# Optimization experiments

Hardware: AMD Instinct MI355X
Metric: run time of the kernel (lower is better)

The kernel has to match this reference:

```python
import jax, jax.numpy as jnp
import numpy as np

# Architecture constants (from module defaults)
D, H, DH, P, G, DEPTH, M, NCLS = 192, 3, 64, 16, 14, 12, 128, 1000  # M = feature_map_dim // 2
EXITS = (4, 8, 12)
TEMP = 1.0 / np.sqrt(DH)  # Favor softmax_temp = 1/sqrt(d_head)
EPS_ATTN = 1e-6           # fast_transformers LinearAttention eps
LN_EPS = 1e-5


def ln(x, g, b):
    mu = x.mean(-1, keepdims=True)
    var = ((x - mu) ** 2).mean(-1, keepdims=True)
    return (x - mu) * jax.lax.rsqrt(var + LN_EPS) * g + b


def favor(x, omega):
    # FAVOR+ positive random features for the softmax kernel.
    # x: [B,L,H,DH], omega: [DH,M] -> phi: [B,L,H,2M]
    xs = x * np.float32(np.sqrt(TEMP))
    off = 0.5 * (xs * xs).sum(-1, keepdims=True)
    u = jnp.einsum('blhd,dm->blhm', xs, omega)
    phi = jnp.concatenate([jnp.exp(u - off), jnp.exp(-u - off)], axis=-1)
    return phi * np.float32(1.0 / np.sqrt(2 * M))


def forward(x, patch_w, patch_b, pe_ln_g, pe_ln_b, cls_token, pos_embed,
            Wq, bq, Wk, bk, Wv, bv, Wo, bo,
            ln1_g, ln1_b, ln2_g, ln2_b, lnb_g, lnb_b,
            W1, b1, W2, b2, omega, head_w, head_b):
    B = x.shape[0]
    # Patch embedding: Conv2d(k=16, s=16) == blocked einsum
    xp = x.reshape(B, 3, G, P, G, P)
    tok = jnp.einsum('bchpwq,dcpq->bhwd', xp, patch_w).reshape(B, G * G, D) + patch_b
    tok = ln(tok, pe_ln_g, pe_ln_b)  # PatchEmbed.norm (norm_layer=LayerNorm)
    tok = jnp.concatenate([jnp.broadcast_to(cls_token, (B, 1, D)), tok], axis=1) + pos_embed
    xc = tok  # [B, 197, D]
    outs = []
    for i in range(DEPTH):
        # --- linear (FAVOR) attention ---
        q = (xc @ Wq[i].T + bq[i]).reshape(B, -1, H, DH)
        k = (xc @ Wk[i].T + bk[i]).reshape(B, -1, H, DH)
        v = (xc @ Wv[i].T + bv[i]).reshape(B, -1, H, DH)
        Qp = favor(q, omega[i])
        Kp = favor(k, omega[i])
        KV = jnp.einsum('bshm,bshd->bhmd', Kp, v)
        Z = 1.0 / (jnp.einsum('blhm,bhm->blh', Qp, Kp.sum(axis=1)) + EPS_ATTN)
        attn = jnp.einsum('blhm,bhmd,blh->blhd', Qp, KV, Z).reshape(B, -1, D)
        # fast_transformers TransformerEncoderLayer (post-norm style)
        xc = xc + attn @ Wo[i].T + bo[i]
        y = xc = ln(xc, ln1_g[i], ln1_b[i])
        y = jax.nn.relu(y @ W1[i].T + b1[i]) @ W2[i].T + b2[i]
        xc = ln(xc + y, ln2_g[i], ln2_b[i])
        # per-block TransformerEncoder final norm (builder final_normalization)
        xc = ln(xc, lnb_g[i], lnb_b[i])
        if (i + 1) in EXITS:
            j = EXITS.index(i + 1)
            z = xc.mean(axis=1)  # AdaptiveAvgPool1d(1) over sequence
            outs.append(z @ head_w[j].T + head_b[j])
    return tuple(outs)


def setup_inputs() -> dict:
    key = jax.random.key(0)
    ks = iter(jax.random.split(key, 32))
    n = lambda shape, s=0.02: jax.random.normal(next(ks), shape, jnp.float32) * s
    return dict(
        x=jax.random.normal(next(ks), (64, 3, 224, 224), jnp.float32),
        patch_w=n((D, 3, P, P)), patch_b=jnp.zeros((D,), jnp.float32),
        pe_ln_g=jnp.ones((D,), jnp.float32), pe_ln_b=jnp.zeros((D,), jnp.float32),
        cls_token=n((1, 1, D)), pos_embed=n((1, G * G + 1, D)),
        Wq=n((DEPTH, D, D)), bq=jnp.zeros((DEPTH, D), jnp.float32),
        Wk=n((DEPTH, D, D)), bk=jnp.zeros((DEPTH, D), jnp.float32),
        Wv=n((DEPTH, D, D)), bv=jnp.zeros((DEPTH, D), jnp.float32),
        Wo=n((DEPTH, D, D)), bo=jnp.zeros((DEPTH, D), jnp.float32),
        ln1_g=jnp.ones((DEPTH, D), jnp.float32), ln1_b=jnp.zeros((DEPTH, D), jnp.float32),
        ln2_g=jnp.ones((DEPTH, D), jnp.float32), ln2_b=jnp.zeros((DEPTH, D), jnp.float32),
        lnb_g=jnp.ones((DEPTH, D), jnp.float32), lnb_b=jnp.zeros((DEPTH, D), jnp.float32),
        W1=n((DEPTH, 4 * D, D)), b1=jnp.zeros((DEPTH, 4 * D), jnp.float32),
        W2=n((DEPTH, D, 4 * D)), b2=jnp.zeros((DEPTH, D), jnp.float32),
        omega=jax.random.normal(next(ks), (DEPTH, DH, M), jnp.float32),
        head_w=n((len(EXITS), NCLS, D)), head_b=jnp.zeros((len(EXITS), NCLS), jnp.float32),
    )


def reference(x, patch_w, patch_b, pe_ln_g, pe_ln_b, cls_token, pos_embed,
              Wq, bq, Wk, bk, Wv, bv, Wo, bo,
              ln1_g, ln1_b, ln2_g, ln2_b, lnb_g, lnb_b,
              W1, b1, W2, b2, omega, head_w, head_b):
    return forward(x, patch_w, patch_b, pe_ln_g, pe_ln_b, cls_token, pos_embed,
                   Wq, bq, Wk, bk, Wv, bv, Wo, bo,
                   ln1_g, ln1_b, ln2_g, ln2_b, lnb_g, lnb_b,
                   W1, b1, W2, b2, omega, head_w, head_b)
```

## Files before the change

kernel.cpp:

```cpp
#include <hip/hip_runtime.h>
#include <math.h>

#define BB     64
#define LLEN   197
#define BLROWS 12608
#define MPAD   12672
#define DMODEL 192
#define NHEAD  3
#define DHEAD  64
#define M2FEAT 256
#define FFDIM  768
#define NDEPTH 12
#define NCLS   1000
#define NPATCH 196
#define BPROWS 12544
#define KPATCH 768
#define PHIRS  264
#define PHTRS  40
#define VLT    208

#define MODE_PLAIN 0
#define MODE_RELU  1
#define MODE_QKV   2

typedef unsigned short ushort;
typedef __attribute__((ext_vector_type(8))) short bf16x8;
typedef __attribute__((ext_vector_type(4))) float floatx4;
typedef __attribute__((ext_vector_type(4))) short short4v;

__device__ __forceinline__ float wave_reduce_sum(float v) {
#pragma unroll
  for (int s = 32; s > 0; s >>= 1) v += __shfl_xor(v, s, 64);
  return v;
}
__device__ __forceinline__ ushort f2bf(float f) {
  unsigned u = __float_as_uint(f);
  return (ushort)((u + 0x7fffu + ((u >> 16) & 1u)) >> 16);
}
__device__ __forceinline__ float bf2f(ushort u) {
  return __uint_as_float(((unsigned)u) << 16);
}
__device__ __forceinline__ void gll16(const ushort* g, ushort* l) {
  __builtin_amdgcn_global_load_lds(
      (const __attribute__((address_space(1))) void*)g,
      (__attribute__((address_space(3))) void*)l, 16, 0, 0);
}

__global__ void zero_buf(uint4* __restrict__ p, int n16) {
  const int i = blockIdx.x * 256 + threadIdx.x;
  if (i < n16) p[i] = uint4{0, 0, 0, 0};
}

__global__ __launch_bounds__(256) void gemm_128(
    const ushort* __restrict__ A, int lda,
    const ushort* __restrict__ W, int ldw,
    const float* __restrict__ bias,
    ushort* __restrict__ C, int ldc, ushort* __restrict__ Vt,
    int Ndim, int Kdim, int mode)
{
  __shared__ __align__(16) ushort As[2][128 * 32];
  __shared__ __align__(16) ushort Ws[2][128 * 32];
  const int tid = threadIdx.x;
  const int bm = blockIdx.x, bn = blockIdx.y;
  const int wave = tid >> 6, lane = tid & 63;
  const int wm = (wave >> 1) * 64, wn = (wave & 1) * 64;
  const int quad = lane >> 4, l16 = lane & 15;
  const int lrow = lane >> 2, lk = (lane & 3) * 8;
  const ushort* Ap = A + (size_t)(bm * 128) * lda;
  const ushort* Wp = W + (size_t)(bn * 128) * ldw;
  floatx4 acc[4][4] = {};
  const int nT = Kdim >> 5;
#pragma unroll
  for (int t = 0; t < 2; ++t) {
    const int rb = (t * 4 + wave) * 16;
    gll16(Ap + (size_t)(rb + lrow) * lda + lk, &As[0][rb * 32]);
    gll16(Wp + (size_t)(rb + lrow) * ldw + lk, &Ws[0][rb * 32]);
  }
  for (int kt = 0; kt < nT; ++kt) {
    const int cur = kt & 1;
    __syncthreads();
    if (kt + 1 < nT) {
      const int kk = (kt + 1) * 32, nxt = cur ^ 1;
#pragma unroll
      for (int t = 0; t < 2; ++t) {
        const int rb = (t * 4 + wave) * 16;
        gll16(Ap + (size_t)(rb + lrow) * lda + kk + lk, &As[nxt][rb * 32]);
        gll16(Wp + (size_t)(rb + lrow) * ldw + kk + lk, &Ws[nxt][rb * 32]);
      }
    }
    bf16x8 af[4], bf[4];
#pragma unroll
    for (int i = 0; i < 4; ++i) {
      af[i] = *(const bf16x8*)&As[cur][(wm + i * 16 + l16) * 32 + quad * 8];
      bf[i] = *(const bf16x8*)&Ws[cur][(wn + i * 16 + l16) * 32 + quad * 8];
    }
#pragma unroll
    for (int i = 0; i < 4; ++i)
#pragma unroll
      for (int j = 0; j < 4; ++j)
        acc[i][j] = __builtin_amdgcn_mfma_f32_16x16x32_bf16(af[i], bf[j], acc[i][j], 0, 0, 0);
  }
  if (mode == MODE_QKV) {
#pragma unroll
    for (int i = 0; i < 4; ++i)
#pragma unroll
      for (int r = 0; r < 4; ++r) {
        const int grow = bm * 128 + wm + i * 16 + quad * 4 + r;
        const int bidx = grow / 197;
        const int lloc = grow - bidx * 197;
#pragma unroll
        for (int j = 0; j < 4; ++j) {
          const int col = bn * 128 + wn + j * 16 + l16;
          if (col >= Ndim) continue;
          const float o = acc[i][j][r] + bias[col];
          if (col < 384) {
            C[(size_t)grow * ldc + col] = f2bf(o);
          } else if (grow < BLROWS) {
            const int h = (col - 384) >> 6, d = (col - 384) & 63;
            Vt[((size_t)(bidx * 3 + h) * 64 + d) * VLT + lloc] = f2bf(o);
          }
        }
      }
  } else {
#pragma unroll
    for (int j = 0; j < 4; ++j) {
      const int col = bn * 128 + wn + j * 16 + l16;
      if (col >= Ndim) continue;
      const float bv = bias[col];
#pragma unroll
      for (int i = 0; i < 4; ++i)
#pragma unroll
        for (int r = 0; r < 4; ++r) {
          const int grow = bm * 128 + wm + i * 16 + quad * 4 + r;
          float o = acc[i][j][r] + bv;
          if (mode == MODE_RELU) o = fmaxf(o, 0.f);
          C[(size_t)grow * ldc + col] = f2bf(o);
        }
    }
  }
}

__global__ __launch_bounds__(256) void gemm_bf2(
    const ushort* __restrict__ A, int lda,
    const ushort* __restrict__ W, int ldw,
    const float* __restrict__ bias,
    ushort* __restrict__ C, int ldc, int Kdim, int mode)
{
  __shared__ __align__(16) ushort As[2][128 * 32];
  __shared__ __align__(16) ushort Ws[2][64 * 32];
  const int tid = threadIdx.x;
  const int bm = blockIdx.x, bn = blockIdx.y;
  const int wave = tid >> 6, lane = tid & 63;
  const int wm = (wave >> 1) * 64, wn = (wave & 1) * 32;
  const int quad = lane >> 4, l16 = lane & 15;
  const int lrow = lane >> 2, lk = (lane & 3) * 8;
  const ushort* Ap = A + (size_t)(bm * 128) * lda;
  const ushort* Wp = W + (size_t)(bn * 64) * ldw;
  floatx4 acc[4][2] = {};
  const int nT = Kdim >> 5;
#pragma unroll
  for (int t = 0; t < 2; ++t) {
    const int rb = (t * 4 + wave) * 16;
    gll16(Ap + (size_t)(rb + lrow) * lda + lk, &As[0][rb * 32]);
  }
  gll16(Wp + (size_t)(wave * 16 + lrow) * ldw + lk, &Ws[0][wave * 16 * 32]);
  for (int kt = 0; kt < nT; ++kt) {
    const int cur = kt & 1;
    __syncthreads();
    if (kt + 1 < nT) {
      const int kk = (kt + 1) * 32, nxt = cur ^ 1;
#pragma unroll
      for (int t = 0; t < 2; ++t) {
        const int rb = (t * 4 + wave) * 16;
        gll16(Ap + (size_t)(rb + lrow) * lda + kk + lk, &As[nxt][rb * 32]);
      }
      gll16(Wp + (size_t)(wave * 16 + lrow) * ldw + kk + lk, &Ws[nxt][wave * 16 * 32]);
    }
    bf16x8 af[4], bf[2];
#pragma unroll
    for (int i = 0; i < 4; ++i)
      af[i] = *(const bf16x8*)&As[cur][(wm + i * 16 + l16) * 32 + quad * 8];
#pragma unroll
    for (int j = 0; j < 2; ++j)
      bf[j] = *(const bf16x8*)&Ws[cur][(wn + j * 16 + l16) * 32 + quad * 8];
#pragma unroll
    for (int i = 0; i < 4; ++i)
#pragma unroll
      for (int j = 0; j < 2; ++j)
        acc[i][j] = __builtin_amdgcn_mfma_f32_16x16x32_bf16(af[i], bf[j], acc[i][j], 0, 0, 0);
  }
#pragma unroll
  for (int j = 0; j < 2; ++j) {
    const int col = bn * 64 + wn + j * 16 + l16;
    const float bv = bias[col];
#pragma unroll
    for (int i = 0; i < 4; ++i)
#pragma unroll
      for (int r = 0; r < 4; ++r) {
        const int grow = bm * 128 + wm + i * 16 + quad * 4 + r;
        float o = acc[i][j][r] + bv;
        if (mode == MODE_RELU) o = fmaxf(o, 0.f);
        C[(size_t)grow * ldc + col] = f2bf(o);
      }
  }
}

__global__ __launch_bounds__(256) void gemm_ln(
    const ushort* __restrict__ A, int lda,
    const ushort* __restrict__ W, int ldw,
    const float* __restrict__ bias,
    ushort* __restrict__ XC,
    const float* __restrict__ ga, const float* __restrict__ ba,
    const float* __restrict__ gb, const float* __restrict__ bb,
    int Kdim, int dln)
{
  __shared__ __align__(16) ushort As[2][64 * 32];
  __shared__ __align__(16) ushort Ws[2][192 * 32];
  const int tid = threadIdx.x;
  const int bm = blockIdx.x;
  const int wave = tid >> 6, lane = tid & 63;
  const int quad = lane >> 4, l16 = lane & 15;
  const int lrow = lane >> 2, lk = (lane & 3) * 8;
  const ushort* Ap = A + (size_t)(bm * 64) * lda;
  floatx4 acc[12] = {};
  const int nT = Kdim >> 5;
  gll16(Ap + (size_t)(wave * 16 + lrow) * lda + lk, &As[0][wave * 16 * 32]);
#pragma unroll
  for (int t = 0; t < 3; ++t) {
    const int rb = wave * 48 + t * 16;
    gll16(W + (size_t)(rb + lrow) * ldw + lk, &Ws[0][rb * 32]);
  }
  for (int kt = 0; kt < nT; ++kt) {
    const int cur = kt & 1;
    __syncthreads();
    if (kt + 1 < nT) {
      const int kk = (kt + 1) * 32, nxt = cur ^ 1;
      gll16(Ap + (size_t)(wave * 16 + lrow) * lda + kk + lk, &As[nxt][wave * 16 * 32]);
#pragma unroll
      for (int t = 0; t < 3; ++t) {
        const int rb = wave * 48 + t * 16;
        gll16(W + (size_t)(rb + lrow) * ldw + kk + lk, &Ws[nxt][rb * 32]);
      }
    }
    const bf16x8 af = *(const bf16x8*)&As[cur][(wave * 16 + l16) * 32 + quad * 8];
#pragma unroll
    for (int j = 0; j < 12; ++j) {
      const bf16x8 bf = *(const bf16x8*)&Ws[cur][(j * 16 + l16) * 32 + quad * 8];
      acc[j] = __builtin_amdgcn_mfma_f32_16x16x32_bf16(af, bf, acc[j], 0, 0, 0);
    }
  }
#pragma unroll
  for (int r = 0; r < 4; ++r) {
    const int row = bm * 64 + wave * 16 + quad * 4 + r;
    ushort* xp = XC + (size_t)row * DMODEL;
    float xr[12];
    float s = 0.f, sq = 0.f;
#pragma unroll
    for (int j = 0; j < 12; ++j) {
      const int col = j * 16 + l16;
      const float o = acc[j][r] + bias[col] + bf2f(xp[col]);
      xr[j] = o; s += o; sq += o * o;
    }
#pragma unroll
    for (int m = 1; m < 16; m <<= 1) {
      s += __shfl_xor(s, m, 64); sq += __shfl_xor(sq, m, 64);
    }
    float mu = s * (1.f / 192.f);
    float var = sq * (1.f / 192.f) - mu * mu;
    float rs = rsqrtf(var + 1e-5f);
#pragma unroll
    for (int j = 0; j < 12; ++j) {
      const int col = j * 16 + l16;
      xr[j] = (xr[j] - mu) * rs * ga[col] + ba[col];
    }
    if (dln) {
      float s2 = 0.f, sq2 = 0.f;
#pragma unroll
      for (int j = 0; j < 12; ++j) { s2 += xr[j]; sq2 += xr[j] * xr[j]; }
#pragma unroll
      for (int m = 1; m < 16; m <<= 1) {
        s2 += __shfl_xor(s2, m, 64); sq2 += __shfl_xor(sq2, m, 64);
      }
      mu = s2 * (1.f / 192.f);
      var = sq2 * (1.f / 192.f) - mu * mu;
      rs = rsqrtf(var + 1e-5f);
#pragma unroll
      for (int j = 0; j < 12; ++j) {
        const int col = j * 16 + l16;
        xr[j] = (xr[j] - mu) * rs * gb[col] + bb[col];
      }
    }
#pragma unroll
    for (int j = 0; j < 12; ++j) xp[j * 16 + l16] = f2bf(xr[j]);
  }
}

__global__ __launch_bounds__(256) void kv_fused(
    const ushort* __restrict__ qkv, const ushort* __restrict__ OmT,
    const ushort* __restrict__ Vt, ushort* __restrict__ KVt)
{
  __shared__ __align__(16) ushort Ks[32 * 64];
  __shared__ __align__(16) ushort Om[64 * 64];
  __shared__ __align__(16) ushort PhT[128 * PHTRS];
  __shared__ __align__(16) ushort Vts[2][64 * 32];
  __shared__ __align__(16) ushort Vcst[16 * 32];
  __shared__ float offs[32];
  const int tid = threadIdx.x;
  const int bh = blockIdx.x, mh = blockIdx.y;
  const int b = bh / 3, h = bh - b * 3;
  const int wave = tid >> 6, lane = tid & 63;
  const int quad = lane >> 4, l16 = lane & 15;
  const int lr8 = lane >> 3, g8 = lane & 7;
  const int lr4 = lane >> 2, g4 = lane & 3;
#pragma unroll
  for (int t = 0; t < 2; ++t) {
    const int rb = (t * 4 + wave) * 8;
    const int row = rb + lr8;
    gll16(OmT + (size_t)(mh * 64 + row) * 64 + ((g8 ^ (row & 7)) * 8), &Om[rb * 64]);
  }
  {
    const int rowK = wave * 8 + lr8;
    gll16(qkv + (size_t)(b * 197 + rowK) * 576 + 192 + h * 64 + ((g8 ^ (rowK & 7)) * 8),
          &Ks[wave * 8 * 64]);
    const int rowV = wave * 16 + lr4;
    gll16(Vt + ((size_t)bh * 64 + rowV) * VLT + ((g4 ^ (rowV & 3)) * 8),
          &Vts[0][wave * 16 * 32]);
  }
  for (int e = tid; e < 16 * 32; e += 256) Vcst[e] = (e < 32) ? 0x3F80 : 0;
  floatx4 acc[2][5] = {};
  for (int c = 0; c < 7; ++c) {
    const int l0 = c * 32;
    const int cur = c & 1;
    __syncthreads();
    if (tid < 64) {
      const int row = tid >> 1, half = tid & 1;
      float s = 0.f;
#pragma unroll
      for (int t = 0; t < 4; ++t) {
        bf16x8 v8 = *(const bf16x8*)&Ks[row * 64 + (((half * 4 + t) ^ (row & 7)) * 8)];
#pragma unroll
        for (int q = 0; q < 8; ++q) { float xv = bf2f((ushort)v8[q]); s += xv * xv; }
      }
      s += __shfl_xor(s, 1, 64);
      if (half == 0) offs[row] = 0.0625f * s;
    }
    floatx4 ui[2] = {};
#pragma unroll
    for (int ksb = 0; ksb < 2; ++ksb) {
      bf16x8 af[2], bfm;
#pragma unroll
      for (int i = 0; i < 2; ++i) {
        const int row = i * 16 + l16;
        af[i] = *(const bf16x8*)&Ks[row * 64 + (((quad + (ksb << 2)) ^ (row & 7)) * 8)];
      }
      {
        const int row = wave * 16 + l16;
        bfm = *(const bf16x8*)&Om[row * 64 + (((quad + (ksb << 2)) ^ (row & 7)) * 8)];
      }
#pragma unroll
      for (int i = 0; i < 2; ++i)
        ui[i] = __builtin_amdgcn_mfma_f32_16x16x32_bf16(af[i], bfm, ui[i], 0, 0, 0);
    }
    __syncthreads();
    {
      const int mloc = wave * 16 + l16;
#pragma unroll
      for (int i = 0; i < 2; ++i) {
#pragma unroll
        for (int r = 0; r < 4; ++r) {
          const int ll = i * 16 + quad * 4 + r;
          float ep = 0.f, em = 0.f;
          if (l0 + ll < 197) {
            const float off = offs[ll];
            const float u = ui[i][r];
            ep = __expf(u - off) * 0.0625f;
            em = __expf(-u - off) * 0.0625f;
          }
          PhT[mloc * PHTRS + ll] = f2bf(ep);
          PhT[(64 + mloc) * PHTRS + ll] = f2bf(em);
        }
      }
    }
    if (c + 1 < 7) {
      const int rowK = wave * 8 + lr8;
      const int lK = (c + 1) * 32 + rowK;
      gll16(qkv + (size_t)(b * 197 + lK) * 576 + 192 + h * 64 + ((g8 ^ (rowK & 7)) * 8),
            &Ks[wave * 8 * 64]);
      const int rowV = wave * 16 + lr4;
      gll16(Vt + ((size_t)bh * 64 + rowV) * VLT + (c + 1) * 32 + ((g4 ^ (rowV & 3)) * 8),
            &Vts[cur ^ 1][wave * 16 * 32]);
    }
    __syncthreads();
    bf16x8 af[2], bf[5];
#pragma unroll
    for (int i = 0; i < 2; ++i)
      af[i] = *(const bf16x8*)&PhT[(wave * 32 + i * 16 + l16) * PHTRS + quad * 8];
#pragma unroll
    for (int j = 0; j < 4; ++j) {
      const int row = j * 16 + l16;
      bf[j] = *(const bf16x8*)&Vts[cur][row * 32 + ((quad ^ (row & 3)) * 8)];
    }
    bf[4] = *(const bf16x8*)&Vcst[l16 * 32 + quad * 8];
#pragma unroll
    for (int i = 0; i < 2; ++i)
#pragma unroll
      for (int j = 0; j < 5; ++j)
        acc[i][j] = __builtin_amdgcn_mfma_f32_16x16x32_bf16(af[i], bf[j], acc[i][j], 0, 0, 0);
  }
#pragma unroll
  for (int i = 0; i < 2; ++i) {
    const int prow0 = wave * 32 + i * 16 + quad * 4;
    const int f0 = (prow0 < 64) ? (mh * 64 + prow0) : (128 + mh * 64 + prow0 - 64);
#pragma unroll
    for (int j = 0; j < 5; ++j) {
      const int d = j * 16 + l16;
      short4v pk;
#pragma unroll
      for (int r = 0; r < 4; ++r) pk[r] = (short)f2bf(acc[i][j][r]);
      *(short4v*)(KVt + ((size_t)bh * 80 + d) * 256 + f0) = pk;
    }
  }
}

__global__ __launch_bounds__(256) void attn_fused(
    const ushort* __restrict__ qkv, const ushort* __restrict__ OmT,
    const ushort* __restrict__ KVt, ushort* __restrict__ OUT)
{
  __shared__ __align__(16) ushort Phi[64 * PHIRS];
  __shared__ __align__(16) ushort Bs[2][80 * 32];
  __shared__ float offs[64];
  __shared__ float zs[64];
  ushort* Qs = Phi;
  ushort* Om = Phi + 64 * 64;
  const int tid = threadIdx.x;
  const int bx = blockIdx.x, bh = blockIdx.y;
  const int b = bh / 3, h = bh - b * 3;
  const int wave = tid >> 6, lane = tid & 63;
  const int quad = lane >> 4, l16 = lane & 15;
  const int lr8 = lane >> 3, g8 = lane & 7;
  const int lr4 = lane >> 2, g4 = lane & 3;
#pragma unroll
  for (int t = 0; t < 2; ++t) {
    const int rb = wave * 16 + t * 8;
    const int row = rb + lr8;
    const int l = bx * 64 + row;
    gll16(qkv + (size_t)(b * 197 + l) * 576 + h * 64 + ((g8 ^ (row & 7)) * 8), &Qs[rb * 64]);
  }
#pragma unroll
  for (int t = 0; t < 4; ++t) {
    const int rb = wave * 32 + t * 8;
    const int row = rb + lr8;
    gll16(OmT + (size_t)row * 64 + ((g8 ^ (row & 7)) * 8), &Om[rb * 64]);
  }
  __syncthreads();
  if (tid < 128) {
    const int row = tid >> 1, half = tid & 1;
    float s = 0.f;
#pragma unroll
    for (int t = 0; t < 4; ++t) {
      bf16x8 v8 = *(const bf16x8*)&Qs[row * 64 + (((half * 4 + t) ^ (row & 7)) * 8)];
#pragma unroll
      for (int q = 0; q < 8; ++q) { float xv = bf2f((ushort)v8[q]); s += xv * xv; }
    }
    s += __shfl_xor(s, 1, 64);
    if (half == 0) offs[row] = 0.0625f * s;
  }
  floatx4 uacc[8] = {};
#pragma unroll
  for (int ksb = 0; ksb < 2; ++ksb) {
    bf16x8 af, bf[8];
    {
      const int row = wave * 16 + l16;
      af = *(const bf16x8*)&Qs[row * 64 + (((quad + (ksb << 2)) ^ (row & 7)) * 8)];
    }
#pragma unroll
    for (int j = 0; j < 8; ++j) {
      const int row = j * 16 + l16;
      bf[j] = *(const bf16x8*)&Om[row * 64 + (((quad + (ksb << 2)) ^ (row & 7)) * 8)];
    }
#pragma unroll
    for (int j = 0; j < 8; ++j)
      uacc[j] = __builtin_amdgcn_mfma_f32_16x16x32_bf16(af, bf[j], uacc[j], 0, 0, 0);
  }
  __syncthreads();
#pragma unroll
  for (int r = 0; r < 4; ++r) {
    const int l = wave * 16 + quad * 4 + r;
    const float off = offs[l];
#pragma unroll
    for (int j = 0; j < 8; ++j) {
      const int m = j * 16 + l16;
      const float u = uacc[j][r];
      Phi[l * PHIRS + m]       = f2bf(__expf(u - off)  * 0.0625f);
      Phi[l * PHIRS + m + 128] = f2bf(__expf(-u - off) * 0.0625f);
    }
  }
  const ushort* Bp = KVt + (size_t)bh * 80 * 256;
  {
    const int row = wave * 16 + lr4;
    gll16(Bp + (size_t)row * 256 + ((g4 ^ (row & 3)) * 8), &Bs[0][wave * 16 * 32]);
    if (wave == 0)
      gll16(Bp + (size_t)(64 + lr4) * 256 + ((g4 ^ (lr4 & 3)) * 8), &Bs[0][64 * 32]);
  }
  floatx4 acc[5] = {};
  for (int c = 0; c < 8; ++c) {
    const int cur = c & 1;
    __syncthreads();
    if (c + 1 < 8) {
      const int m0 = (c + 1) * 32, nxt = cur ^ 1;
      const int row = wave * 16 + lr4;
      gll16(Bp + (size_t)row * 256 + m0 + ((g4 ^ (row & 3)) * 8), &Bs[nxt][wave * 16 * 32]);
      if (wave == 0)
        gll16(Bp + (size_t)(64 + lr4) * 256 + m0 + ((g4 ^ (lr4 & 3)) * 8), &Bs[nxt][64 * 32]);
    }
    const int m0 = c * 32;
    bf16x8 af, bf[5];
    af = *(const bf16x8*)&Phi[(wave * 16 + l16) * PHIRS + m0 + quad * 8];
#pragma unroll
    for (int j = 0; j < 5; ++j) {
      const int row = j * 16 + l16;
      bf[j] = *(const bf16x8*)&Bs[cur][row * 32 + ((quad ^ (row & 3)) * 8)];
    }
#pragma unroll
    for (int j = 0; j < 5; ++j)
      acc[j] = __builtin_amdgcn_mfma_f32_16x16x32_bf16(af, bf[j], acc[j], 0, 0, 0);
  }
  if (l16 == 0) {
#pragma unroll
    for (int r = 0; r < 4; ++r)
      zs[wave * 16 + quad * 4 + r] = acc[4][r];
  }
  __syncthreads();
#pragma unroll
  for (int r = 0; r < 4; ++r) {
    const int ll = wave * 16 + quad * 4 + r;
    const int l = bx * 64 + ll;
    if (l >= 197) continue;
    const float z = 1.f / (zs[ll] + 1e-6f);
#pragma unroll
    for (int j = 0; j < 4; ++j)
      OUT[(size_t)(b * 197 + l) * 192 + h * 64 + j * 16 + l16] =
          f2bf(acc[j][r] * z);
  }
}

__global__ void conv_qkv(const float* __restrict__ Wq, const float* __restrict__ Wk,
                         const float* __restrict__ Wv, const float* __restrict__ bq,
                         const float* __restrict__ bk, const float* __restrict__ bv,
                         ushort* __restrict__ dst, float* __restrict__ bdst) {
  const int l = blockIdx.y;
  const int e = blockIdx.x * 256 + threadIdx.x;
  const int n = e / 192, k = e - n * 192;
  const float* src;
  if (n < 192)      src = Wq + (size_t)l * 36864 + n * 192;
  else if (n < 384) src = Wk + (size_t)l * 36864 + (n - 192) * 192;
  else              src = Wv + (size_t)l * 36864 + (n - 384) * 192;
  dst[(size_t)l * 640 * 192 + e] = f2bf(src[k]);
  if (e < 576) {
    float bvv;
    if (e < 192)      bvv = bq[l * 192 + e];
    else if (e < 384) bvv = bk[l * 192 + e - 192];
    else              bvv = bv[l * 192 + e - 384];
    bdst[l * 576 + e] = bvv;
  }
}

__global__ void conv_pad(const float* __restrict__ src, ushort* __restrict__ dst,
                         int NK, int padNK) {
  const int l = blockIdx.y;
  const int e = blockIdx.x * 256 + threadIdx.x;
  if (e < NK) dst[(size_t)l * padNK + e] = f2bf(src[(size_t)l * NK + e]);
}

__global__ void conv_omt(const float* __restrict__ om, ushort* __restrict__ dst) {
  const int l = blockIdx.y;
  const int e = blockIdx.x * 256 + threadIdx.x;
  const int m = e >> 6, d = e & 63;
  dst[(size_t)l * 8192 + e] = f2bf(0.35355339059327379f * om[(size_t)l * 8192 + d * 128 + m]);
}

__global__ __launch_bounds__(256) void im2col_kernel(
    const float* __restrict__ X, ushort* __restrict__ Apd)
{
  const int bp = blockIdx.x;
  const int b = bp / NPATCH, p = bp - b * NPATCH;
  const int gh = p / 14, gw = p - gh * 14;
  for (int e = threadIdx.x; e < KPATCH; e += 256) {
    const int c = e >> 8, rem = e & 255, ph = rem >> 4, pw = rem & 15;
    Apd[(size_t)bp * KPATCH + e] =
        f2bf(X[((size_t)(b * 3 + c) * 224 + gh * 16 + ph) * 224 + gw * 16 + pw]);
  }
}

__global__ __launch_bounds__(256) void assemble_kernel(
    const ushort* __restrict__ TK, const float* __restrict__ g,
    const float* __restrict__ bt, const float* __restrict__ cls,
    const float* __restrict__ pos, ushort* __restrict__ XC)
{
  const int w = threadIdx.x >> 6, lane = threadIdx.x & 63;
  const int row = blockIdx.x * 4 + w;
  const int b = row / LLEN, l = row - b * LLEN;
  float o0, o1, o2;
  if (l == 0) {
    o0 = cls[lane]; o1 = cls[lane + 64]; o2 = cls[lane + 128];
  } else {
    const ushort* tp = TK + (size_t)(b * NPATCH + l - 1) * DMODEL;
    const float x0 = bf2f(tp[lane]), x1 = bf2f(tp[lane + 64]), x2 = bf2f(tp[lane + 128]);
    const float s  = wave_reduce_sum(x0 + x1 + x2);
    const float sq = wave_reduce_sum(x0 * x0 + x1 * x1 + x2 * x2);
    const float mu = s * (1.f / 192.f);
    const float var = sq * (1.f / 192.f) - mu * mu;
    const float rs = rsqrtf(var + 1e-5f);
    o0 = (x0 - mu) * rs * g[lane]       + bt[lane];
    o1 = (x1 - mu) * rs * g[lane + 64]  + bt[lane + 64];
    o2 = (x2 - mu) * rs * g[lane + 128] + bt[lane + 128];
  }
  o0 += pos[l * DMODEL + lane];
  o1 += pos[l * DMODEL + lane + 64];
  o2 += pos[l * DMODEL + lane + 128];
  ushort* xp = XC + (size_t)row * DMODEL;
  xp[lane] = f2bf(o0); xp[lane + 64] = f2bf(o1); xp[lane + 128] = f2bf(o2);
}

__global__ __launch_bounds__(192) void pool_kernel(
    const ushort* __restrict__ XC, float* __restrict__ Zp)
{
  const int b = blockIdx.x, d = threadIdx.x;
  float s = 0.f;
#pragma unroll 4
  for (int l = 0; l < LLEN; ++l) s += bf2f(XC[(size_t)(b * LLEN + l) * DMODEL + d]);
  Zp[b * DMODEL + d] = s * (1.f / 197.f);
}

__global__ __launch_bounds__(256) void head_kernel(
    const float* __restrict__ Zp, const float* __restrict__ HW,
    const float* __restrict__ HB, float* __restrict__ OUTp)
{
  const int n = blockIdx.x * 256 + threadIdx.x;
  const int b = blockIdx.y;
  if (n < NCLS) {
    const float* z = Zp + b * DMODEL;
    const float* w = HW + (size_t)n * DMODEL;
    float s = HB[n];
#pragma unroll 4
    for (int d = 0; d < DMODEL; ++d) s = fmaf(z[d], w[d], s);
    OUTp[(size_t)b * NCLS + n] = s;
  }
}

extern "C" void kernel_launch(void* const* d_in, const int* in_sizes, int n_in,
                              void* d_out, int out_size, void* d_ws, size_t ws_size,
                              hipStream_t stream) {
  const float* x        = (const float*)d_in[0];
  const float* patch_w  = (const float*)d_in[1];
  const float* patch_b  = (const float*)d_in[2];
  const float* pe_ln_g  = (const float*)d_in[3];
  const float* pe_ln_b  = (const float*)d_in[4];
  const float* cls_tok  = (const float*)d_in[5];
  const float* pos_emb  = (const float*)d_in[6];
  const float* Wq = (const float*)d_in[7];
  const float* bq = (const float*)d_in[8];
  const float* Wk = (const float*)d_in[9];
  const float* bk = (const float*)d_in[10];
  const float* Wv = (const float*)d_in[11];
  const float* bv = (const float*)d_in[12];
  const float* Wo = (const float*)d_in[13];
  const float* bo = (const float*)d_in[14];
  const float* ln1_g = (const float*)d_in[15];
  const float* ln1_b = (const float*)d_in[16];
  const float* ln2_g = (const float*)d_in[17];
  const float* ln2_b = (const float*)d_in[18];
  const float* lnb_g = (const float*)d_in[19];
  const float* lnb_b = (const float*)d_in[20];
  const float* W1 = (const float*)d_in[21];
  const float* b1 = (const float*)d_in[22];
  const float* W2 = (const float*)d_in[23];
  const float* b2 = (const float*)d_in[24];
  const float* omega  = (const float*)d_in[25];
  const float* head_w = (const float*)d_in[26];
  const float* head_b = (const float*)d_in[27];
  float* out = (float*)d_out;
  char* wsb = (char*)d_ws;

  size_t off = 0;
  auto carve = [&](size_t bytes) { size_t o = off; off += (bytes + 255) & ~(size_t)255; return o; };
  ushort* xc     = (ushort*)(wsb + carve((size_t)MPAD * 192 * 2));
  ushort* qkv    = (ushort*)(wsb + carve((size_t)MPAD * 576 * 2));
  ushort* ab     = (ushort*)(wsb + carve((size_t)MPAD * 192 * 2));
  ushort* hidden = (ushort*)(wsb + carve((size_t)MPAD * 768 * 2));
  ushort* KVt    = (ushort*)(wsb + carve((size_t)192 * 80 * 256 * 2));
  ushort* Vt     = (ushort*)(wsb + carve((size_t)192 * 64 * VLT * 2 + 1024));
  float*  ZPb    = (float*)(wsb + carve((size_t)64 * 192 * 4));
  float*  bqkv   = (float*)(wsb + carve((size_t)12 * 576 * 4));
  ushort* Wqkv_bf = (ushort*)(wsb + carve((size_t)12 * 640 * 192 * 2));
  ushort* Wo_bf   = (ushort*)(wsb + carve((size_t)12 * 256 * 192 * 2));
  ushort* W1_bf   = (ushort*)(wsb + carve((size_t)12 * 768 * 192 * 2));
  ushort* W2_bf   = (ushort*)(wsb + carve((size_t)12 * 256 * 768 * 2));
  ushort* Wp_bf   = (ushort*)(wsb + carve((size_t)256 * 768 * 2));
  ushort* Om_bf   = (ushort*)(wsb + carve((size_t)12 * 128 * 64 * 2));
  ushort* i2c     = hidden;

  {
    const int n16 = (int)(((size_t)192 * 64 * VLT * 2 + 1024) / 16);
    zero_buf<<<(n16 + 255) / 256, 256, 0, stream>>>((uint4*)Vt, n16);
  }

  conv_qkv<<<dim3(432, 12), 256, 0, stream>>>(Wq, Wk, Wv, bq, bk, bv, Wqkv_bf, bqkv);
  conv_pad<<<dim3(144, 12), 256, 0, stream>>>(Wo, Wo_bf, 36864, 256 * 192);
  conv_pad<<<dim3(576, 12), 256, 0, stream>>>(W1, W1_bf, 147456, 768 * 192);
  conv_pad<<<dim3(576, 12), 256, 0, stream>>>(W2, W2_bf, 147456, 256 * 768);
  conv_pad<<<dim3(576, 1), 256, 0, stream>>>(patch_w, Wp_bf, 147456, 256 * 768);
  conv_omt<<<dim3(32, 12), 256, 0, stream>>>(omega, Om_bf);

  im2col_kernel<<<BPROWS, 256, 0, stream>>>(x, i2c);
  gemm_bf2<<<dim3(98, 3), 256, 0, stream>>>(i2c, KPATCH, Wp_bf, KPATCH,
      patch_b, ab, DMODEL, KPATCH, MODE_PLAIN);
  assemble_kernel<<<BLROWS / 4, 256, 0, stream>>>(ab, pe_ln_g, pe_ln_b,
                                                  cls_tok, pos_emb, xc);

  const int exits[3] = {3, 7, 11};
  for (int i = 0; i < NDEPTH; ++i) {
    gemm_128<<<dim3(99, 5), 256, 0, stream>>>(xc, DMODEL,
        Wqkv_bf + (size_t)i * 640 * 192, DMODEL, bqkv + i * 576,
        qkv, 576, Vt, 576, DMODEL, MODE_QKV);
    kv_fused<<<dim3(192, 2), 256, 0, stream>>>(qkv,
        Om_bf + (size_t)i * 8192, Vt, KVt);
    attn_fused<<<dim3(4, 192), 256, 0, stream>>>(qkv,
        Om_bf + (size_t)i * 8192, KVt, ab);
    gemm_ln<<<MPAD / 64, 256, 0, stream>>>(ab, DMODEL,
        Wo_bf + (size_t)i * 256 * 192, DMODEL, bo + i * DMODEL, xc,
        ln1_g + i * DMODEL, ln1_b + i * DMODEL, nullptr, nullptr,
        DMODEL, 0);
    gemm_128<<<dim3(99, 6), 256, 0, stream>>>(xc, DMODEL,
        W1_bf + (size_t)i * 768 * 192, DMODEL, b1 + i * FFDIM,
        hidden, FFDIM, nullptr, FFDIM, DMODEL, MODE_RELU);
    gemm_ln<<<MPAD / 64, 256, 0, stream>>>(hidden, FFDIM,
        W2_bf + (size_t)i * 256 * 768, FFDIM, b2 + i * DMODEL, xc,
        ln2_g + i * DMODEL, ln2_b + i * DMODEL,
        lnb_g + i * DMODEL, lnb_b + i * DMODEL,
        FFDIM, 1);

    for (int j = 0; j < 3; ++j) {
      if (i == exits[j]) {
        pool_kernel<<<BB, 192, 0, stream>>>(xc, ZPb);
        head_kernel<<<dim3(4, BB), 256, 0, stream>>>(
            ZPb, head_w + (size_t)j * NCLS * DMODEL, head_b + (size_t)j * NCLS,
            out + (size_t)j * BB * NCLS);
      }
    }
  }
}
```

Measured before the change: 1.611 ms.

## Double GEMM K-tile to 64 with XOR-swizzled LDS and fuse pooling into head

```diff
diff --git a/kernel.cpp b/kernel.cpp
--- a/kernel.cpp
+++ b/kernel.cpp
@@ -58,47 +58,52 @@
     ushort* __restrict__ C, int ldc, ushort* __restrict__ Vt,
     int Ndim, int Kdim, int mode)
 {
-  __shared__ __align__(16) ushort As[2][128 * 32];
-  __shared__ __align__(16) ushort Ws[2][128 * 32];
+  __shared__ __align__(16) ushort As[2][128 * 64];
+  __shared__ __align__(16) ushort Ws[2][128 * 64];
   const int tid = threadIdx.x;
   const int bm = blockIdx.x, bn = blockIdx.y;
   const int wave = tid >> 6, lane = tid & 63;
   const int wm = (wave >> 1) * 64, wn = (wave & 1) * 64;
   const int quad = lane >> 4, l16 = lane & 15;
-  const int lrow = lane >> 2, lk = (lane & 3) * 8;
+  const int srow = lane >> 3;
+  const int scol = ((lane & 7) ^ srow) * 8;
   const ushort* Ap = A + (size_t)(bm * 128) * lda;
   const ushort* Wp = W + (size_t)(bn * 128) * ldw;
   floatx4 acc[4][4] = {};
-  const int nT = Kdim >> 5;
-#pragma unroll
-  for (int t = 0; t < 2; ++t) {
-    const int rb = (t * 4 + wave) * 16;
-    gll16(Ap + (size_t)(rb + lrow) * lda + lk, &As[0][rb * 32]);
-    gll16(Wp + (size_t)(rb + lrow) * ldw + lk, &Ws[0][rb * 32]);
+  const int nT = Kdim >> 6;
+#pragma unroll
+  for (int t = 0; t < 4; ++t) {
+    const int rb = (t * 4 + wave) * 8;
+    gll16(Ap + (size_t)(rb + srow) * lda + scol, &As[0][rb * 64]);
+    gll16(Wp + (size_t)(rb + srow) * ldw + scol, &Ws[0][rb * 64]);
   }
   for (int kt = 0; kt < nT; ++kt) {
     const int cur = kt & 1;
     __syncthreads();
     if (kt + 1 < nT) {
-      const int kk = (kt + 1) * 32, nxt = cur ^ 1;
-#pragma unroll
-      for (int t = 0; t < 2; ++t) {
-        const int rb = (t * 4 + wave) * 16;
-        gll16(Ap + (size_t)(rb + lrow) * lda + kk + lk, &As[nxt][rb * 32]);
-        gll16(Wp + (size_t)(rb + lrow) * ldw + kk + lk, &Ws[nxt][rb * 32]);
-      }
-    }
-    bf16x8 af[4], bf[4];
-#pragma unroll
-    for (int i = 0; i < 4; ++i) {
-      af[i] = *(const bf16x8*)&As[cur][(wm + i * 16 + l16) * 32 + quad * 8];
-      bf[i] = *(const bf16x8*)&Ws[cur][(wn + i * 16 + l16) * 32 + quad * 8];
-    }
-#pragma unroll
-    for (int i = 0; i < 4; ++i)
-#pragma unroll
-      for (int j = 0; j < 4; ++j)
-        acc[i][j] = __builtin_amdgcn_mfma_f32_16x16x32_bf16(af[i], bf[j], acc[i][j], 0, 0, 0);
+      const int kk = (kt + 1) * 64, nxt = cur ^ 1;
+#pragma unroll
+      for (int t = 0; t < 4; ++t) {
+        const int rb = (t * 4 + wave) * 8;
+        gll16(Ap + (size_t)(rb + srow) * lda + kk + scol, &As[nxt][rb * 64]);
+        gll16(Wp + (size_t)(rb + srow) * ldw + kk + scol, &Ws[nxt][rb * 64]);
+      }
+    }
+#pragma unroll
+    for (int ks = 0; ks < 2; ++ks) {
+      bf16x8 af[4], bf[4];
+#pragma unroll
+      for (int i = 0; i < 4; ++i) {
+        const int ra = wm + i * 16 + l16, rw = wn + i * 16 + l16;
+        af[i] = *(const bf16x8*)&As[cur][ra * 64 + ((((ks << 2) | quad) ^ (ra & 7)) * 8)];
+        bf[i] = *(const bf16x8*)&Ws[cur][rw * 64 + ((((ks << 2) | quad) ^ (rw & 7)) * 8)];
+      }
+#pragma unroll
+      for (int i = 0; i < 4; ++i)
+#pragma unroll
+        for (int j = 0; j < 4; ++j)
+          acc[i][j] = __builtin_amdgcn_mfma_f32_16x16x32_bf16(af[i], bf[j], acc[i][j], 0, 0, 0);
+    }
   }
   if (mode == MODE_QKV) {
 #pragma unroll
@@ -146,48 +151,64 @@
     const float* __restrict__ bias,
     ushort* __restrict__ C, int ldc, int Kdim, int mode)
 {
-  __shared__ __align__(16) ushort As[2][128 * 32];
-  __shared__ __align__(16) ushort Ws[2][64 * 32];
+  __shared__ __align__(16) ushort As[2][128 * 64];
+  __shared__ __align__(16) ushort Ws[2][64 * 64];
   const int tid = threadIdx.x;
   const int bm = blockIdx.x, bn = blockIdx.y;
   const int wave = tid >> 6, lane = tid & 63;
   const int wm = (wave >> 1) * 64, wn = (wave & 1) * 32;
   const int quad = lane >> 4, l16 = lane & 15;
-  const int lrow = lane >> 2, lk = (lane & 3) * 8;
+  const int srow = lane >> 3;
+  const int scol = ((lane & 7) ^ srow) * 8;
   const ushort* Ap = A + (size_t)(bm * 128) * lda;
   const ushort* Wp = W + (size_t)(bn * 64) * ldw;
   floatx4 acc[4][2] = {};
-  const int nT = Kdim >> 5;
+  const int nT = Kdim >> 6;
+#pragma unroll
+  for (int t = 0; t < 4; ++t) {
+    const int rb = (t * 4 + wave) * 8;
+    gll16(Ap + (size_t)(rb + srow) * lda + scol, &As[0][rb * 64]);
+  }
 #pragma unroll
   for (int t = 0; t < 2; ++t) {
-    const int rb = (t * 4 + wave) * 16;
-    gll16(Ap + (size_t)(rb + lrow) * lda + lk, &As[0][rb * 32]);
-  }
-  gll16(Wp + (size_t)(wave * 16 + lrow) * ldw + lk, &Ws[0][wave * 16 * 32]);
+    const int rb = (t * 4 + wave) * 8;
+    gll16(Wp + (size_t)(rb + srow) * ldw + scol, &Ws[0][rb * 64]);
+  }
   for (int kt = 0; kt < nT; ++kt) {
     const int cur = kt & 1;
     __syncthreads();
     if (kt + 1 < nT) {
-      const int kk = (kt + 1) * 32, nxt = cur ^ 1;
+      const int kk = (kt + 1) * 64, nxt = cur ^ 1;
+#pragma unroll
+      for (int t = 0; t < 4; ++t) {
+        const int rb = (t * 4 + wave) * 8;
+        gll16(Ap + (size_t)(rb + srow) * lda + kk + scol, &As[nxt][rb * 64]);
+      }
 #pragma unroll
       for (int t = 0; t < 2; ++t) {
-        const int rb = (t * 4 + wave) * 16;
-        gll16(Ap + (size_t)(rb + lrow) * lda + kk + lk, &As[nxt][rb * 32]);
-      }
-      gll16(Wp + (size_t)(wave * 16 + lrow) * ldw + kk + lk, &Ws[nxt][wave * 16 * 32]);
-    }
-    bf16x8 af[4], bf[2];
-#pragma unroll
-    for (int i = 0; i < 4; ++i)
-      af[i] = *(const bf16x8*)&As[cur][(wm + i * 16 + l16) * 32 + quad * 8];
-#pragma unroll
-    for (int j = 0; j < 2; ++j)
-      bf[j] = *(const bf16x8*)&Ws[cur][(wn + j * 16 + l16) * 32 + quad * 8];
-#pragma unroll
-    for (int i = 0; i < 4; ++i)
-#pragma unroll
-      for (int j = 0; j < 2; ++j)
-        acc[i][j] = __builtin_amdgcn_mfma_f32_16x16x32_bf16(af[i], bf[j], acc[i][j], 0, 0, 0);
+        const int rb = (t * 4 + wave) * 8;
+        gll16(Wp + (size_t)(rb + srow) * ldw + kk + scol, &Ws[nxt][rb * 64]);
+      }
+    }
+#pragma unroll
+    for (int ks = 0; ks < 2; ++ks) {
+      bf16x8 af[4], bf[2];
+#pragma unroll
+      for (int i = 0; i < 4; ++i) {
+        const int ra = wm + i * 16 + l16;
+        af[i] = *(const bf16x8*)&As[cur][ra * 64 + ((((ks << 2) | quad) ^ (ra & 7)) * 8)];
+      }
+#pragma unroll
+      for (int j = 0; j < 2; ++j) {
+        const int rw = wn + j * 16 + l16;
+        bf[j] = *(const bf16x8*)&Ws[cur][rw * 64 + ((((ks << 2) | quad) ^ (rw & 7)) * 8)];
+      }
+#pragma unroll
+      for (int i = 0; i < 4; ++i)
+#pragma unroll
+        for (int j = 0; j < 2; ++j)
+          acc[i][j] = __builtin_amdgcn_mfma_f32_16x16x32_bf16(af[i], bf[j], acc[i][j], 0, 0, 0);
+    }
   }
 #pragma unroll
   for (int j = 0; j < 2; ++j) {
@@ -214,39 +235,53 @@
     const float* __restrict__ gb, const float* __restrict__ bb,
     int Kdim, int dln)
 {
-  __shared__ __align__(16) ushort As[2][64 * 32];
-  __shared__ __align__(16) ushort Ws[2][192 * 32];
+  __shared__ __align__(16) ushort As[2][64 * 64];
+  __shared__ __align__(16) ushort Ws[2][192 * 64];
   const int tid = threadIdx.x;
   const int bm = blockIdx.x;
   const int wave = tid >> 6, lane = tid & 63;
   const int quad = lane >> 4, l16 = lane & 15;
-  const int lrow = lane >> 2, lk = (lane & 3) * 8;
+  const int srow = lane >> 3;
+  const int scol = ((lane & 7) ^ srow) * 8;
   const ushort* Ap = A + (size_t)(bm * 64) * lda;
   floatx4 acc[12] = {};
-  const int nT = Kdim >> 5;
-  gll16(Ap + (size_t)(wave * 16 + lrow) * lda + lk, &As[0][wave * 16 * 32]);
-#pragma unroll
-  for (int t = 0; t < 3; ++t) {
-    const int rb = wave * 48 + t * 16;
-    gll16(W + (size_t)(rb + lrow) * ldw + lk, &Ws[0][rb * 32]);
+  const int nT = Kdim >> 6;
+#pragma unroll
+  for (int t = 0; t < 2; ++t) {
+    const int rb = (t * 4 + wave) * 8;
+    gll16(Ap + (size_t)(rb + srow) * lda + scol, &As[0][rb * 64]);
+  }
+#pragma unroll
+  for (int t = 0; t < 6; ++t) {
+    const int rb = (t * 4 + wave) * 8;
+    gll16(W + (size_t)(rb + srow) * ldw + scol, &Ws[0][rb * 64]);
   }
   for (int kt = 0; kt < nT; ++kt) {
     const int cur = kt & 1;
     __syncthreads();
     if (kt + 1 < nT) {
-      const int kk = (kt + 1) * 32, nxt = cur ^ 1;
-      gll16(Ap + (size_t)(wave * 16 + lrow) * lda + kk + lk, &As[nxt][wave * 16 * 32]);
-#pragma unroll
-      for (int t = 0; t < 3; ++t) {
-        const int rb = wave * 48 + t * 16;
-        gll16(W + (size_t)(rb + lrow) * ldw + kk + lk, &Ws[nxt][rb * 32]);
-      }
-    }
-    const bf16x8 af = *(const bf16x8*)&As[cur][(wave * 16 + l16) * 32 + quad * 8];
-#pragma unroll
-    for (int j = 0; j < 12; ++j) {
-      const bf16x8 bf = *(const bf16x8*)&Ws[cur][(j * 16 + l16) * 32 + quad * 8];
-      acc[j] = __builtin_amdgcn_mfma_f32_16x16x32_bf16(af, bf, acc[j], 0, 0, 0);
+      const int kk = (kt + 1) * 64, nxt = cur ^ 1;
+#pragma unroll
+      for (int t = 0; t < 2; ++t) {
+        const int rb = (t * 4 + wave) * 8;
+        gll16(Ap + (size_t)(rb + srow) * lda + kk + scol, &As[nxt][rb * 64]);
+      }
+#pragma unroll
+      for (int t = 0; t < 6; ++t) {
+        const int rb = (t * 4 + wave) * 8;
+        gll16(W + (size_t)(rb + srow) * ldw + kk + scol, &Ws[nxt][rb * 64]);
+      }
+    }
+#pragma unroll
+    for (int ks = 0; ks < 2; ++ks) {
+      const int ra = wave * 16 + l16;
+      const bf16x8 af = *(const bf16x8*)&As[cur][ra * 64 + ((((ks << 2) | quad) ^ (ra & 7)) * 8)];
+#pragma unroll
+      for (int j = 0; j < 12; ++j) {
+        const int rw = j * 16 + l16;
+        const bf16x8 bf = *(const bf16x8*)&Ws[cur][rw * 64 + ((((ks << 2) | quad) ^ (rw & 7)) * 8)];
+        acc[j] = __builtin_amdgcn_mfma_f32_16x16x32_bf16(af, bf, acc[j], 0, 0, 0);
+      }
     }
   }
 #pragma unroll
@@ -622,28 +657,29 @@
   xp[lane] = f2bf(o0); xp[lane + 64] = f2bf(o1); xp[lane + 128] = f2bf(o2);
 }
 
-__global__ __launch_bounds__(192) void pool_kernel(
-    const ushort* __restrict__ XC, float* __restrict__ Zp)
-{
-  const int b = blockIdx.x, d = threadIdx.x;
-  float s = 0.f;
-#pragma unroll 4
-  for (int l = 0; l < LLEN; ++l) s += bf2f(XC[(size_t)(b * LLEN + l) * DMODEL + d]);
-  Zp[b * DMODEL + d] = s * (1.f / 197.f);
-}
-
 __global__ __launch_bounds__(256) void head_kernel(
-    const float* __restrict__ Zp, const float* __restrict__ HW,
+    const ushort* __restrict__ XC, const float* __restrict__ HW,
     const float* __restrict__ HB, float* __restrict__ OUTp)
 {
-  const int n = blockIdx.x * 256 + threadIdx.x;
+  __shared__ float zsh[DMODEL];
   const int b = blockIdx.y;
+  const int tid = threadIdx.x;
+  const int wave = tid >> 6, lane = tid & 63;
+  if (wave < 3) {
+    const int d = wave * 64 + lane;
+    const ushort* xp = XC + (size_t)b * LLEN * DMODEL + d;
+    float s = 0.f;
+#pragma unroll 4
+    for (int l = 0; l < LLEN; ++l) s += bf2f(xp[(size_t)l * DMODEL]);
+    zsh[d] = s * (1.f / 197.f);
+  }
+  __syncthreads();
+  const int n = blockIdx.x * 256 + tid;
   if (n < NCLS) {
-    const float* z = Zp + b * DMODEL;
     const float* w = HW + (size_t)n * DMODEL;
     float s = HB[n];
 #pragma unroll 4
-    for (int d = 0; d < DMODEL; ++d) s = fmaf(z[d], w[d], s);
+    for (int d = 0; d < DMODEL; ++d) s = fmaf(zsh[d], w[d], s);
     OUTp[(size_t)b * NCLS + n] = s;
   }
 }
@@ -690,7 +726,6 @@
   ushort* hidden = (ushort*)(wsb + carve((size_t)MPAD * 768 * 2));
   ushort* KVt    = (ushort*)(wsb + carve((size_t)192 * 80 * 256 * 2));
   ushort* Vt     = (ushort*)(wsb + carve((size_t)192 * 64 * VLT * 2 + 1024));
-  float*  ZPb    = (float*)(wsb + carve((size_t)64 * 192 * 4));
   float*  bqkv   = (float*)(wsb + carve((size_t)12 * 576 * 4));
   ushort* Wqkv_bf = (ushort*)(wsb + carve((size_t)12 * 640 * 192 * 2));
   ushort* Wo_bf   = (ushort*)(wsb + carve((size_t)12 * 256 * 192 * 2));
@@ -742,9 +777,8 @@
 
     for (int j = 0; j < 3; ++j) {
       if (i == exits[j]) {
-        pool_kernel<<<BB, 192, 0, stream>>>(xc, ZPb);
         head_kernel<<<dim3(4, BB), 256, 0, stream>>>(
-            ZPb, head_w + (size_t)j * NCLS * DMODEL, head_b + (size_t)j * NCLS,
+            xc, head_w + (size_t)j * NCLS * DMODEL, head_b + (size_t)j * NCLS,
             out + (size_t)j * BB * NCLS);
       }
     }
```

After: 1.491 ms. -7.5%, faster.
